# Optimization experiments

Measured on AMD Instinct MI355X. Metric: run time of the kernel, lower is better.

Reference implementation:

```python
import jax, jax.numpy as jnp
import numpy as np

N = 50000      # nodes
E = 800000     # edges
F_IN = 16      # feature_size
D = 96         # d_model
G = 64         # graphs per batch


def _gcn_conv(x, W, b, src, dst, dis, num_nodes):
    # PyG GCNConv: out = D^{-1/2}(A+I)D^{-1/2} X W + b (self-loops already in src/dst)
    h = x @ W                                   # [N, out]
    norm = (dis[src] * dis[dst])[:, None]       # [E+N, 1]
    msg = h[src] * norm                         # gather + scale
    agg = jax.ops.segment_sum(msg, dst, num_segments=num_nodes)
    return agg + b


def _forward(x, W_init, b_init, W1, b1, W2, b2, W3, b3, W4, b4,
             Wo1, bo1, Wo2, bo2, edge_index, batch_index):
    act = jax.nn.leaky_relu  # default negative_slope=0.01, matches nn.LeakyReLU()
    n = x.shape[0]
    # add self-loops once; degree includes self-loop (PyG gcn_norm default)
    loop = jnp.arange(n, dtype=edge_index.dtype)
    src = jnp.concatenate([edge_index[0], loop])
    dst = jnp.concatenate([edge_index[1], loop])
    deg = jax.ops.segment_sum(jnp.ones_like(src, dtype=x.dtype), dst, num_segments=n)
    dis = jax.lax.rsqrt(deg)  # deg >= 1 due to self-loops

    h = act(_gcn_conv(x, W_init, b_init, src, dst, dis, n))
    h = act(_gcn_conv(h, W1, b1, src, dst, dis, n))
    h = act(_gcn_conv(h, W2, b2, src, dst, dis, n))
    h = act(_gcn_conv(h, W3, b3, src, dst, dis, n))
    h = act(_gcn_conv(h, W4, b4, src, dst, dis, n))

    # global max + mean pooling per graph
    gmax = jax.ops.segment_max(h, batch_index, num_segments=G)
    gsum = jax.ops.segment_sum(h, batch_index, num_segments=G)
    cnt = jax.ops.segment_sum(jnp.ones((n,), dtype=h.dtype), batch_index, num_segments=G)
    gmean = gsum / jnp.maximum(cnt, 1.0)[:, None]
    pooled = jnp.concatenate([gmax, gmean], axis=1)  # [G, 2D]

    out = act(pooled @ Wo1 + bo1)  # dropout is identity in eval
    out = out @ Wo2 + bo2          # [G, 1]
    return out


def setup_inputs() -> dict:
    key = jax.random.key(0)
    ks = jax.random.split(key, 16)
    def glorot(k, shape):
        lim = float(np.sqrt(6.0 / (shape[0] + shape[1])))
        return jax.random.uniform(k, shape, jnp.float32, -lim, lim)
    inp = {
        'x': jax.random.normal(ks[0], (N, F_IN), jnp.float32),
        'edge_index': jax.random.randint(ks[1], (2, E), 0, N, dtype=jnp.int64),
        'batch_index': jnp.sort(jax.random.randint(ks[2], (N,), 0, G, dtype=jnp.int64)),
        'W_init': glorot(ks[3], (F_IN, D)), 'b_init': jnp.zeros((D,), jnp.float32),
        'W1': glorot(ks[4], (D, D)), 'b1': jnp.zeros((D,), jnp.float32),
        'W2': glorot(ks[5], (D, D)), 'b2': jnp.zeros((D,), jnp.float32),
        'W3': glorot(ks[6], (D, D)), 'b3': jnp.zeros((D,), jnp.float32),
        'W4': glorot(ks[7], (D, D)), 'b4': jnp.zeros((D,), jnp.float32),
        'Wo1': glorot(ks[8], (2 * D, D)), 'bo1': jnp.zeros((D,), jnp.float32),
        'Wo2': glorot(ks[9], (D, 1)), 'bo2': jnp.zeros((1,), jnp.float32),
    }
    return inp


def reference(x, edge_index, batch_index, W_init, b_init, W1, b1, W2, b2,
              W3, b3, W4, b4, Wo1, bo1, Wo2, bo2):
    return _forward(x, W_init, b_init, W1, b1, W2, b2, W3, b3, W4, b4,
                    Wo1, bo1, Wo2, bo2, edge_index, batch_index)
```

## Files before the change

### kernel.cpp

```cpp
#include <hip/hip_runtime.h>
#include <hip/hip_fp16.h>
#include <math.h>

#define LEAKY(x) ((x) > 0.f ? (x) : 0.01f * (x))
#define BK_SHIFT 9
#define NBMAX 128
#define BCAP 16384
#define EPAD 64

typedef _Float16 half8 __attribute__((ext_vector_type(8)));
typedef float f32x4 __attribute__((ext_vector_type(4)));

#define FMIX_LO(acc, u, m) \
    asm("v_fma_mix_f32 %0, %1, %2, %0 op_sel:[0,0,0] op_sel_hi:[1,0,0]" \
        : "+v"(acc) : "v"(u), "v"(m))
#define FMIX_HI(acc, u, m) \
    asm("v_fma_mix_f32 %0, %1, %2, %0 op_sel:[1,0,0] op_sel_hi:[1,0,0]" \
        : "+v"(acc) : "v"(u), "v"(m))

__device__ __forceinline__ void acc12(float (&acc)[12], uint2 u0, uint2 u1,
                                      uint2 u2, float m) {
    FMIX_LO(acc[0], u0.x, m);  FMIX_HI(acc[1], u0.x, m);
    FMIX_LO(acc[2], u0.y, m);  FMIX_HI(acc[3], u0.y, m);
    FMIX_LO(acc[4], u1.x, m);  FMIX_HI(acc[5], u1.x, m);
    FMIX_LO(acc[6], u1.y, m);  FMIX_HI(acc[7], u1.y, m);
    FMIX_LO(acc[8], u2.x, m);  FMIX_HI(acc[9], u2.x, m);
    FMIX_LO(acc[10], u2.y, m); FMIX_HI(acc[11], u2.y, m);
}

__device__ __forceinline__ unsigned encf(float f) {
    unsigned u = __float_as_uint(f);
    return (u & 0x80000000u) ? ~u : (u | 0x80000000u);
}
__device__ __forceinline__ float decf(unsigned u) {
    if (u == 0u) return -INFINITY;
    unsigned b = (u & 0x80000000u) ? (u & 0x7fffffffu) : ~u;
    return __uint_as_float(b);
}

__global__ __launch_bounds__(256) void prep(const float* __restrict__ W1,
                                            const float* __restrict__ W2,
                                            const float* __restrict__ W3,
                                            const float* __restrict__ W4,
                                            _Float16* __restrict__ WtG,
                                            int* __restrict__ bfill,
                                            int* __restrict__ epad,
                                            unsigned* __restrict__ gmaxU,
                                            float* __restrict__ gsum, int G) {
    int bi = blockIdx.x, tid = threadIdx.x;
    if (bi < 4) {
        const float* W = bi == 0 ? W1 : bi == 1 ? W2 : bi == 2 ? W3 : W4;
        _Float16* dst = WtG + bi * 9216;
        for (int idx = tid; idx < 9216; idx += 256) {
            int k = idx / 96, nn = idx % 96;
            dst[nn * 96 + k] = (_Float16)W[idx];
        }
    } else if (bi == 4) {
        for (int i2 = tid; i2 < NBMAX; i2 += 256) bfill[i2] = 0;
        for (int i2 = tid; i2 < EPAD; i2 += 256) epad[i2] = 0;
    } else if (bi == 5) {
        for (int i2 = tid; i2 < G * 96; i2 += 256) gmaxU[i2] = 0u;
    } else {
        for (int i2 = tid; i2 < G * 96; i2 += 256) gsum[i2] = 0.f;
    }
}

__global__ __launch_bounds__(256) void bin_kernel(const int* __restrict__ src,
                                                  const int* __restrict__ dst,
                                                  int* __restrict__ bfill,
                                                  uint2* __restrict__ tmp,
                                                  int E, int nb) {
    __shared__ int hist[NBMAX];
    __shared__ int scanbuf[NBMAX];
    __shared__ int lofs[NBMAX];
    __shared__ int adj[NBMAX];
    __shared__ uint2 buf[2048];
    __shared__ unsigned char bkt_of[2048];
    int base = blockIdx.x * 2048;
    int cnt = min(2048, E - base);
    int tid = threadIdx.x;
    for (int b = tid; b < NBMAX; b += 256) hist[b] = 0;
    __syncthreads();
    int es[8], ed[8];
#pragma unroll
    for (int k = 0; k < 8; ++k) {
        int l = tid + k * 256;
        if (l < cnt) {
            es[k] = src[base + l];
            ed[k] = dst[base + l];
            atomicAdd(&hist[ed[k] >> BK_SHIFT], 1);
        }
    }
    __syncthreads();
    if (tid < NBMAX) scanbuf[tid] = hist[tid];
    __syncthreads();
    for (int off = 1; off < NBMAX; off <<= 1) {
        int t = (tid < NBMAX && tid >= off) ? scanbuf[tid - off] : 0;
        __syncthreads();
        if (tid < NBMAX) scanbuf[tid] += t;
        __syncthreads();
    }
    if (tid < nb) {
        int cb = hist[tid];
        int start = scanbuf[tid] - cb;
        lofs[tid] = start;
        int g = (cb > 0) ? atomicAdd(&bfill[tid], cb) : 0;
        adj[tid] = tid * BCAP + g - start;
    }
    __syncthreads();
#pragma unroll
    for (int k = 0; k < 8; ++k) {
        int l = tid + k * 256;
        if (l < cnt) {
            int b = ed[k] >> BK_SHIFT;
            int r = atomicAdd(&lofs[b], 1);
            buf[r] = make_uint2((unsigned)es[k], (unsigned)ed[k]);
            bkt_of[r] = (unsigned char)b;
        }
    }
    __syncthreads();
    for (int j = tid; j < cnt; j += 256) {
        int b = bkt_of[j];
        tmp[adj[b] + j] = buf[j];
    }
}

__global__ __launch_bounds__(512) void place2(const uint2* __restrict__ tmp,
                                              const int* __restrict__ bfill,
                                              const float* __restrict__ X,
                                              float* __restrict__ dis,
                                              int* __restrict__ row_ptr,
                                              int* __restrict__ edge_src,
                                              float* __restrict__ Z0, int kq,
                                              int n, int E, int nb) {
    __shared__ int hist[512];
    __shared__ int sc[512];
    __shared__ int sbf[NBMAX];
    __shared__ int bb_s;
    int b = blockIdx.x;
    int tid = threadIdx.x;
    if (tid < NBMAX) sbf[tid] = (tid < nb) ? bfill[tid] : 0;
    hist[tid] = 0;
    __syncthreads();
    if (tid == 0) {
        int s = 0;
        for (int k = 0; k < b; ++k) s += sbf[k];
        bb_s = s;
    }
    __syncthreads();
    int bb = bb_s;
    int cnt = sbf[b];
    const uint2* mybkt = tmp + (size_t)b * BCAP;
    int node0 = b << BK_SHIFT;
    for (int j = tid; j < cnt; j += 512)
        atomicAdd(&hist[(int)mybkt[j].y - node0], 1);
    __syncthreads();
    int v = hist[tid];
    sc[tid] = v;
    __syncthreads();
    for (int off = 1; off < 512; off <<= 1) {
        int t = (tid >= off) ? sc[tid - off] : 0;
        __syncthreads();
        sc[tid] += t;
        __syncthreads();
    }
    int excl = sc[tid] - v;
    int i = node0 + tid;
    if (i < n) {
        row_ptr[i] = bb + excl;
        float di = rsqrtf((float)(v + 1));
        dis[i] = di;
        const float4* X4 = (const float4*)X;
        float4* Z4 = (float4*)Z0;
        for (int j = 0; j < kq; ++j) {
            float4 xv = X4[(size_t)i * kq + j];
            Z4[(size_t)i * kq + j] = make_float4(di * xv.x, di * xv.y, di * xv.z, di * xv.w);
        }
    }
    if (b == 0 && tid == 0) row_ptr[n] = E;
    __syncthreads();
    hist[tid] = bb + excl;
    __syncthreads();
    for (int j = tid; j < cnt; j += 512) {
        uint2 ev = mybkt[j];
        int pos = atomicAdd(&hist[(int)ev.y - node0], 1);
        edge_src[pos] = (int)ev.x;
    }
}

__global__ __launch_bounds__(256) void agg_wave0(const float* __restrict__ Z,
                                                 const float* __restrict__ dis,
                                                 const int* __restrict__ row_ptr,
                                                 const int* __restrict__ edge_src,
                                                 float* __restrict__ A, int n) {
    int i = (blockIdx.x * 256 + threadIdx.x) >> 6;
    if (i >= n) return;
    int lane = threadIdx.x & 63;
    int g = lane >> 2;
    int c = lane & 3;
    const float4* Z4 = (const float4*)Z;
    float di = dis[i];
    size_t base = (size_t)i * 4 + c;
    float4 acc = (g == 0) ? Z4[base] : make_float4(0.f, 0.f, 0.f, 0.f);
    int re0 = row_ptr[i], re1 = row_ptr[i + 1];
    int e0 = re0 + g;
    int s0 = edge_src[e0];
    int s1 = edge_src[e0 + 16];
    float m0 = (e0 < re1) ? 1.f : 0.f;
    float m1 = (e0 + 16 < re1) ? 1.f : 0.f;
    float4 u0 = Z4[(size_t)s0 * 4 + c];
    float4 u1 = Z4[(size_t)s1 * 4 + c];
    acc.x = fmaf(u0.x, m0, acc.x); acc.y = fmaf(u0.y, m0, acc.y);
    acc.z = fmaf(u0.z, m0, acc.z); acc.w = fmaf(u0.w, m0, acc.w);
    acc.x = fmaf(u1.x, m1, acc.x); acc.y = fmaf(u1.y, m1, acc.y);
    acc.z = fmaf(u1.z, m1, acc.z); acc.w = fmaf(u1.w, m1, acc.w);
    for (int e = e0 + 32; e < re1; e += 16) {
        int s = edge_src[e];
        float4 u = Z4[(size_t)s * 4 + c];
        acc.x += u.x; acc.y += u.y; acc.z += u.z; acc.w += u.w;
    }
#pragma unroll
    for (int m = 4; m < 64; m <<= 1) {
        acc.x += __shfl_xor(acc.x, m);
        acc.y += __shfl_xor(acc.y, m);
        acc.z += __shfl_xor(acc.z, m);
        acc.w += __shfl_xor(acc.w, m);
    }
    if (g == 0)
        ((float4*)A)[base] = make_float4(di * acc.x, di * acc.y,
                                         di * acc.z, di * acc.w);
}

__global__ __launch_bounds__(256) void agg_wave_h(const __half* __restrict__ Zh,
                                                  const float* __restrict__ dis,
                                                  const int* __restrict__ row_ptr,
                                                  const int* __restrict__ edge_src,
                                                  __half* __restrict__ A, int n) {
    int i = (blockIdx.x * 256 + threadIdx.x) >> 6;
    if (i >= n) return;
    int lane = threadIdx.x & 63;
    int g = lane >> 3;
    int c = lane & 7;
    float di = dis[i];
    float acc[12];
#pragma unroll
    for (int k = 0; k < 12; ++k) acc[k] = 0.f;
    int re0 = row_ptr[i], re1 = row_ptr[i + 1];
    int e0 = re0 + g;
    int s[4]; float m[4];
#pragma unroll
    for (int k = 0; k < 4; ++k) {
        int e = e0 + k * 8;
        s[k] = edge_src[e];
        m[k] = (e < re1) ? 1.0f : 0.0f;
    }
    uint2 u[4][3];
#pragma unroll
    for (int k = 0; k < 4; ++k) {
        const uint2* zp = (const uint2*)(Zh + (size_t)s[k] * 96 + c * 12);
        u[k][0] = zp[0]; u[k][1] = zp[1]; u[k][2] = zp[2];
    }
    if (g == 0) {
        const uint2* zp = (const uint2*)(Zh + (size_t)i * 96 + c * 12);
        acc12(acc, zp[0], zp[1], zp[2], 1.0f);
    }
#pragma unroll
    for (int k = 0; k < 4; ++k) acc12(acc, u[k][0], u[k][1], u[k][2], m[k]);
    for (int e = e0 + 32; e < re1; e += 8) {
        int s2 = edge_src[e];
        const uint2* zp = (const uint2*)(Zh + (size_t)s2 * 96 + c * 12);
        acc12(acc, zp[0], zp[1], zp[2], 1.0f);
    }
#pragma unroll
    for (int m2 = 8; m2 < 64; m2 <<= 1) {
#pragma unroll
        for (int k = 0; k < 12; ++k) acc[k] += __shfl_xor(acc[k], m2);
    }
    if (g == 0) {
        __half2 h0 = __floats2half2_rn(di * acc[0], di * acc[1]);
        __half2 h1 = __floats2half2_rn(di * acc[2], di * acc[3]);
        __half2 h2 = __floats2half2_rn(di * acc[4], di * acc[5]);
        __half2 h3 = __floats2half2_rn(di * acc[6], di * acc[7]);
        __half2 h4 = __floats2half2_rn(di * acc[8], di * acc[9]);
        __half2 h5 = __floats2half2_rn(di * acc[10], di * acc[11]);
        uint2 o0, o1, o2;
        o0.x = *(unsigned*)&h0; o0.y = *(unsigned*)&h1;
        o1.x = *(unsigned*)&h2; o1.y = *(unsigned*)&h3;
        o2.x = *(unsigned*)&h4; o2.y = *(unsigned*)&h5;
        uint2* ap = (uint2*)(A + (size_t)i * 96 + c * 12);
        ap[0] = o0; ap[1] = o1; ap[2] = o2;
    }
}

template <bool SCALE>
__global__ __launch_bounds__(256) void gemm_mfma(const __half* __restrict__ A,
                                                 const _Float16* __restrict__ Wt,
                                                 const float* __restrict__ b,
                                                 const float* __restrict__ dis,
                                                 __half* __restrict__ Xn, int n) {
    int tid = threadIdx.x;
    int i0 = blockIdx.x * 64;
    int w = tid >> 6, lane = tid & 63;
    int q = lane >> 4, c = lane & 15;
    int arow = i0 + w * 16 + c;
    const _Float16* Ap = (const _Float16*)A;
    half8 af[3];
    if (arow < n) {
#pragma unroll
        for (int kc = 0; kc < 3; ++kc)
            af[kc] = *(const half8*)&Ap[(size_t)arow * 96 + kc * 32 + q * 8];
    } else {
#pragma unroll
        for (int kc = 0; kc < 3; ++kc)
#pragma unroll
            for (int j = 0; j < 8; ++j) af[kc][j] = (_Float16)0.f;
    }
    float dvals[4];
#pragma unroll
    for (int r = 0; r < 4; ++r) {
        int gi = i0 + w * 16 + q * 4 + r;
        dvals[r] = (SCALE && gi < n) ? dis[gi] : 1.f;
    }
#pragma unroll
    for (int nt = 0; nt < 6; ++nt) {
        f32x4 acc = {0.f, 0.f, 0.f, 0.f};
#pragma unroll
        for (int kc = 0; kc < 3; ++kc) {
            half8 bf = *(const half8*)&Wt[(size_t)(nt * 16 + c) * 96 + kc * 32 + q * 8];
            acc = __builtin_amdgcn_mfma_f32_16x16x32_f16(af[kc], bf, acc, 0, 0, 0);
        }
        int col = nt * 16 + c;
        float bias = b[col];
#pragma unroll
        for (int r = 0; r < 4; ++r) {
            int gi = i0 + w * 16 + q * 4 + r;
            if (gi < n) {
                float v = acc[r] + bias;
                v = LEAKY(v);
                if (SCALE) v *= dvals[r];
                ((_Float16*)Xn)[(size_t)gi * 96 + col] = (_Float16)v;
            }
        }
    }
}

__global__ __launch_bounds__(256) void gemm_pool(const __half* __restrict__ A,
                                                 const _Float16* __restrict__ Wt,
                                                 const float* __restrict__ b,
                                                 const int* __restrict__ batch,
                                                 unsigned* __restrict__ gmaxU,
                                                 float* __restrict__ gsum, int n) {
    __shared__ float pmaxs[4][96];
    __shared__ float psums[4][96];
    int tid = threadIdx.x;
    int i0 = blockIdx.x * 64;
    int w = tid >> 6, lane = tid & 63;
    int q = lane >> 4, c = lane & 15;
    int arow = i0 + w * 16 + c;
    const _Float16* Ap = (const _Float16*)A;
    half8 af[3];
    if (arow < n) {
#pragma unroll
        for (int kc = 0; kc < 3; ++kc)
            af[kc] = *(const half8*)&Ap[(size_t)arow * 96 + kc * 32 + q * 8];
    } else {
#pragma unroll
        for (int kc = 0; kc < 3; ++kc)
#pragma unroll
            for (int j = 0; j < 8; ++j) af[kc][j] = (_Float16)0.f;
    }
    int row0 = i0 + w * 16;
    bool wuni = (row0 + 15 < n) && (batch[row0] == batch[row0 + 15]);
    bool buni = (i0 + 63 < n) && (batch[i0] == batch[i0 + 63]);
    int gw = wuni ? batch[row0] : 0;
#pragma unroll
    for (int nt = 0; nt < 6; ++nt) {
        f32x4 acc = {0.f, 0.f, 0.f, 0.f};
#pragma unroll
        for (int kc = 0; kc < 3; ++kc) {
            half8 bf = *(const half8*)&Wt[(size_t)(nt * 16 + c) * 96 + kc * 32 + q * 8];
            acc = __builtin_amdgcn_mfma_f32_16x16x32_f16(af[kc], bf, acc, 0, 0, 0);
        }
        int col = nt * 16 + c;
        float bias = b[col];
        float v[4];
#pragma unroll
        for (int r = 0; r < 4; ++r) {
            float t = acc[r] + bias;
            v[r] = LEAKY(t);
        }
        if (wuni) {
            float mx = fmaxf(fmaxf(v[0], v[1]), fmaxf(v[2], v[3]));
            float sm = v[0] + v[1] + v[2] + v[3];
            mx = fmaxf(mx, __shfl_xor(mx, 16)); sm += __shfl_xor(sm, 16);
            mx = fmaxf(mx, __shfl_xor(mx, 32)); sm += __shfl_xor(sm, 32);
            if (buni) {
                if (q == 0) { pmaxs[w][col] = mx; psums[w][col] = sm; }
            } else if (q == 0) {
                atomicMax(&gmaxU[gw * 96 + col], encf(mx));
                atomicAdd(&gsum[gw * 96 + col], sm);
            }
        } else {
            int r = 0;
            while (r < 4) {
                int gi = i0 + w * 16 + q * 4 + r;
                if (gi >= n) break;
                int gb = batch[gi];
                float mx = v[r], sm = v[r];
                int r2 = r + 1;
                for (; r2 < 4; ++r2) {
                    int gi2 = i0 + w * 16 + q * 4 + r2;
                    if (gi2 >= n || batch[gi2] != gb) break;
                    mx = fmaxf(mx, v[r2]); sm += v[r2];
                }
                atomicMax(&gmaxU[gb * 96 + col], encf(mx));
                atomicAdd(&gsum[gb * 96 + col], sm);
                r = r2;
            }
        }
    }
    __syncthreads();
    if (buni && tid < 96) {
        float m = fmaxf(fmaxf(pmaxs[0][tid], pmaxs[1][tid]),
                        fmaxf(pmaxs[2][tid], pmaxs[3][tid]));
        float s = psums[0][tid] + psums[1][tid] + psums[2][tid] + psums[3][tid];
        int gb = batch[i0];
        atomicMax(&gmaxU[gb * 96 + tid], encf(m));
        atomicAdd(&gsum[gb * 96 + tid], s);
    }
}

__global__ __launch_bounds__(192) void gemm_l0(const float* __restrict__ A,
                                               const float* __restrict__ W,
                                               const float* __restrict__ b,
                                               const float* __restrict__ dis,
                                               __half* __restrict__ Xn, int n) {
    constexpr int KQ = 4;
    __shared__ __align__(16) float4 Al[64 * KQ];
    int tid = threadIdx.x;
    int i0 = blockIdx.x * 64;
    for (int idx = tid; idx < 64 * KQ; idx += 192) {
        int gi = i0 + idx / KQ;
        Al[idx] = (gi < n) ? ((const float4*)A)[(size_t)i0 * KQ + idx]
                           : make_float4(0.f, 0.f, 0.f, 0.f);
    }
    __syncthreads();
    int fq = tid % 24;
    int g = tid / 24;
    const float4* W4 = (const float4*)W;
    float4 bb = ((const float4*)b)[fq];
    float4 acc[8];
#pragma unroll
    for (int r = 0; r < 8; ++r) acc[r] = bb;
    for (int kc = 0; kc < 16; kc += 8) {
        float4 w[8];
#pragma unroll
        for (int kk = 0; kk < 8; ++kk) w[kk] = W4[(size_t)(kc + kk) * 24 + fq];
#pragma unroll
        for (int r = 0; r < 8; ++r) {
            const float4* ar = &Al[(g * 8 + r) * KQ + (kc >> 2)];
#pragma unroll
            for (int k4 = 0; k4 < 2; ++k4) {
                float4 a = ar[k4];
                float4 w0 = w[4 * k4 + 0], w1 = w[4 * k4 + 1];
                float4 w2 = w[4 * k4 + 2], w3 = w[4 * k4 + 3];
                acc[r].x += a.x * w0.x + a.y * w1.x + a.z * w2.x + a.w * w3.x;
                acc[r].y += a.x * w0.y + a.y * w1.y + a.z * w2.y + a.w * w3.y;
                acc[r].z += a.x * w0.z + a.y * w1.z + a.z * w2.z + a.w * w3.z;
                acc[r].w += a.x * w0.w + a.y * w1.w + a.z * w2.w + a.w * w3.w;
            }
        }
    }
#pragma unroll
    for (int r = 0; r < 8; ++r) {
        int gi = i0 + g * 8 + r;
        if (gi < n) {
            float di = dis[gi];
            float4 o;
            o.x = di * LEAKY(acc[r].x); o.y = di * LEAKY(acc[r].y);
            o.z = di * LEAKY(acc[r].z); o.w = di * LEAKY(acc[r].w);
            __half2 h0 = __floats2half2_rn(o.x, o.y);
            __half2 h1 = __floats2half2_rn(o.z, o.w);
            uint2 u;
            u.x = *(unsigned*)&h0;
            u.y = *(unsigned*)&h1;
            ((uint2*)Xn)[(size_t)gi * 24 + fq] = u;
        }
    }
}

__device__ __forceinline__ int lower_bound(const int* b, int n, int v) {
    int lo = 0, hi = n;
    while (lo < hi) {
        int m = (lo + hi) >> 1;
        if (b[m] < v) lo = m + 1; else hi = m;
    }
    return lo;
}

__global__ void pool_final(const unsigned* __restrict__ gmaxU,
                           const float* __restrict__ gsum,
                           const int* __restrict__ batch,
                           const float* __restrict__ Wo1, const float* __restrict__ bo1,
                           const float* __restrict__ Wo2, const float* __restrict__ bo2,
                           float* __restrict__ out, int n) {
    __shared__ float pooled[192];
    __shared__ float sh[96];
    int g = blockIdx.x, f = threadIdx.x;
    int s = lower_bound(batch, n, g), e = lower_bound(batch, n, g + 1);
    float cnt = fmaxf((float)(e - s), 1.f);
    pooled[f] = decf(gmaxU[(size_t)g * 96 + f]);
    pooled[96 + f] = gsum[(size_t)g * 96 + f] / cnt;
    __syncthreads();
    float acc = bo1[f];
    for (int k = 0; k < 192; ++k) acc += pooled[k] * Wo1[k * 96 + f];
    float a = LEAKY(acc);
    sh[f] = a * Wo2[f];
    __syncthreads();
    if (f == 0) {
        float sacc = 0.f;
        for (int k = 0; k < 96; ++k) sacc += sh[k];
        out[g] = sacc + bo2[0];
    }
}

extern "C" void kernel_launch(void* const* d_in, const int* in_sizes, int n_in,
                              void* d_out, int out_size, void* d_ws, size_t ws_size,
                              hipStream_t stream) {
    const float* x      = (const float*)d_in[0];
    const int*   eidx   = (const int*)d_in[1];
    const int*   batch  = (const int*)d_in[2];
    const float* W_init = (const float*)d_in[3];
    const float* b_init = (const float*)d_in[4];
    const float* W1 = (const float*)d_in[5];  const float* b1 = (const float*)d_in[6];
    const float* W2 = (const float*)d_in[7];  const float* b2 = (const float*)d_in[8];
    const float* W3 = (const float*)d_in[9];  const float* b3 = (const float*)d_in[10];
    const float* W4 = (const float*)d_in[11]; const float* b4 = (const float*)d_in[12];
    const float* Wo1 = (const float*)d_in[13]; const float* bo1 = (const float*)d_in[14];
    const float* Wo2 = (const float*)d_in[15]; const float* bo2 = (const float*)d_in[16];
    float* out = (float*)d_out;

    const int N = in_sizes[2];
    const int E = in_sizes[1] / 2;
    const int G = out_size;
    const int* src = eidx;
    const int* dst = eidx + E;

    const int nbBkt  = (N + (1 << BK_SHIFT) - 1) >> BK_SHIFT;

    char* ws = (char*)d_ws;
    size_t off = 0;
    auto alloc = [&](size_t bytes) {
        size_t o = off;
        off += (bytes + 255) & ~(size_t)255;
        return o;
    };
    float*    dis      = (float*)(ws + alloc((size_t)N * 4));
    int*      row_ptr  = (int*)(ws + alloc((size_t)(N + 1) * 4));
    int*      bfill    = (int*)(ws + alloc(NBMAX * 4));
    unsigned* gmaxU    = (unsigned*)(ws + alloc((size_t)G * 96 * 4));
    float*    gsumB    = (float*)(ws + alloc((size_t)G * 96 * 4));
    int*      edge_src = (int*)(ws + alloc((size_t)(E + EPAD) * 4));
    float*    Z0       = (float*)(ws + alloc((size_t)N * 16 * 4));
    __half*   ZA       = (__half*)(ws + alloc((size_t)N * 96 * 2));
    __half*   ZB       = (__half*)(ws + alloc((size_t)N * 96 * 2));
    __half*   AggH     = (__half*)(ws + alloc((size_t)N * 96 * 2));
    float*    Agg0     = (float*)(ws + alloc((size_t)N * 16 * 4));
    _Float16* WtG      = (_Float16*)(ws + alloc((size_t)4 * 9216 * 2));
    uint2*    tmp      = (uint2*)(ws + alloc((size_t)nbBkt * BCAP * 8));
    (void)ws_size; (void)n_in;

    const int nbWave = (N + 3) / 4;
    const int nbTile = (N + 63) / 64;

    prep<<<7, 256, 0, stream>>>(W1, W2, W3, W4, WtG, bfill, edge_src + E,
                                gmaxU, gsumB, G);
    bin_kernel<<<(E + 2047) / 2048, 256, 0, stream>>>(src, dst, bfill, tmp, E, nbBkt);
    place2<<<nbBkt, 512, 0, stream>>>(tmp, bfill, x, dis, row_ptr, edge_src, Z0,
                                      4, N, E, nbBkt);

    agg_wave0<<<nbWave, 256, 0, stream>>>(Z0, dis, row_ptr, edge_src, Agg0, N);
    gemm_l0<<<nbTile, 192, 0, stream>>>(Agg0, W_init, b_init, dis, ZA, N);

    const float* bs[4] = {b1, b2, b3, b4};
    __half* cur = ZA;
    __half* nxt = ZB;
    for (int l = 0; l < 4; ++l) {
        agg_wave_h<<<nbWave, 256, 0, stream>>>(cur, dis, row_ptr, edge_src, AggH, N);
        if (l < 3) {
            gemm_mfma<true><<<nbTile, 256, 0, stream>>>(AggH, WtG + l * 9216, bs[l],
                                                        dis, nxt, N);
            __half* t = cur; cur = nxt; nxt = t;
        } else {
            gemm_pool<<<nbTile, 256, 0, stream>>>(AggH, WtG + 3 * 9216, bs[3],
                                                  batch, gmaxU, gsumB, N);
        }
    }

    pool_final<<<G, 96, 0, stream>>>(gmaxU, gsumB, batch, Wo1, bo1, Wo2, bo2, out, N);
}
```

Before: 327.0 us.

## Split fp16 node features into three 32-column planes for aggregation

Stores the 96-wide fp16 node features as three planes of 32 columns, so each aggregation launch handles one plane per block. Each lane now gathers one 8-byte chunk instead of three, and the GEMM and layer-0 kernels read and write the planar layout. The aim is a smaller per-row gather footprint that fits cache better, plus more blocks in flight. The cost is that row_ptr and edge_src are read three times, along with three times as many edge iterations. Out-of-range edge indices are also clamped to re0 so masked lanes no longer read past the row.

```diff
diff --git a/kernel.cpp b/kernel.cpp
--- a/kernel.cpp
+++ b/kernel.cpp
@@ -18,14 +18,9 @@
     asm("v_fma_mix_f32 %0, %1, %2, %0 op_sel:[1,0,0] op_sel_hi:[1,0,0]" \
         : "+v"(acc) : "v"(u), "v"(m))
 
-__device__ __forceinline__ void acc12(float (&acc)[12], uint2 u0, uint2 u1,
-                                      uint2 u2, float m) {
-    FMIX_LO(acc[0], u0.x, m);  FMIX_HI(acc[1], u0.x, m);
-    FMIX_LO(acc[2], u0.y, m);  FMIX_HI(acc[3], u0.y, m);
-    FMIX_LO(acc[4], u1.x, m);  FMIX_HI(acc[5], u1.x, m);
-    FMIX_LO(acc[6], u1.y, m);  FMIX_HI(acc[7], u1.y, m);
-    FMIX_LO(acc[8], u2.x, m);  FMIX_HI(acc[9], u2.x, m);
-    FMIX_LO(acc[10], u2.y, m); FMIX_HI(acc[11], u2.y, m);
+__device__ __forceinline__ void acc4(float (&acc)[4], uint2 u, float m) {
+    FMIX_LO(acc[0], u.x, m); FMIX_HI(acc[1], u.x, m);
+    FMIX_LO(acc[2], u.y, m); FMIX_HI(acc[3], u.y, m);
 }
 
 __device__ __forceinline__ unsigned encf(float f) {
@@ -204,8 +199,10 @@
     float4 acc = (g == 0) ? Z4[base] : make_float4(0.f, 0.f, 0.f, 0.f);
     int re0 = row_ptr[i], re1 = row_ptr[i + 1];
     int e0 = re0 + g;
-    int s0 = edge_src[e0];
-    int s1 = edge_src[e0 + 16];
+    int ec0 = (e0 < re1) ? e0 : re0;
+    int ec1 = (e0 + 16 < re1) ? e0 + 16 : re0;
+    int s0 = edge_src[ec0];
+    int s1 = edge_src[ec1];
     float m0 = (e0 < re1) ? 1.f : 0.f;
     float m1 = (e0 + 16 < re1) ? 1.f : 0.f;
     float4 u0 = Z4[(size_t)s0 * 4 + c];
@@ -231,64 +228,57 @@
                                          di * acc.z, di * acc.w);
 }
 
-__global__ __launch_bounds__(256) void agg_wave_h(const __half* __restrict__ Zh,
-                                                  const float* __restrict__ dis,
-                                                  const int* __restrict__ row_ptr,
-                                                  const int* __restrict__ edge_src,
-                                                  __half* __restrict__ A, int n) {
-    int i = (blockIdx.x * 256 + threadIdx.x) >> 6;
+__global__ __launch_bounds__(256) void agg_wave_hp(const __half* __restrict__ Zh,
+                                                   const float* __restrict__ dis,
+                                                   const int* __restrict__ row_ptr,
+                                                   const int* __restrict__ edge_src,
+                                                   __half* __restrict__ A,
+                                                   int n, int nbw) {
+    int bi = blockIdx.x;
+    int plane = bi / nbw;
+    int wi = bi - plane * nbw;
+    int i = (wi * 256 + threadIdx.x) >> 6;
     if (i >= n) return;
     int lane = threadIdx.x & 63;
     int g = lane >> 3;
     int c = lane & 7;
+    const uint2* Zp = (const uint2*)Zh + (size_t)plane * n * 8;
+    uint2* Ap = (uint2*)A + (size_t)plane * n * 8;
     float di = dis[i];
-    float acc[12];
-#pragma unroll
-    for (int k = 0; k < 12; ++k) acc[k] = 0.f;
+    float acc[4];
+#pragma unroll
+    for (int k = 0; k < 4; ++k) acc[k] = 0.f;
     int re0 = row_ptr[i], re1 = row_ptr[i + 1];
     int e0 = re0 + g;
     int s[4]; float m[4];
 #pragma unroll
     for (int k = 0; k < 4; ++k) {
         int e = e0 + k * 8;
-        s[k] = edge_src[e];
+        int ec = (e < re1) ? e : re0;
+        s[k] = edge_src[ec];
         m[k] = (e < re1) ? 1.0f : 0.0f;
     }
-    uint2 u[4][3];
-#pragma unroll
-    for (int k = 0; k < 4; ++k) {
-        const uint2* zp = (const uint2*)(Zh + (size_t)s[k] * 96 + c * 12);
-        u[k][0] = zp[0]; u[k][1] = zp[1]; u[k][2] = zp[2];
-    }
-    if (g == 0) {
-        const uint2* zp = (const uint2*)(Zh + (size_t)i * 96 + c * 12);
-        acc12(acc, zp[0], zp[1], zp[2], 1.0f);
-    }
-#pragma unroll
-    for (int k = 0; k < 4; ++k) acc12(acc, u[k][0], u[k][1], u[k][2], m[k]);
+    uint2 u[4];
+#pragma unroll
+    for (int k = 0; k < 4; ++k) u[k] = Zp[(size_t)s[k] * 8 + c];
+    if (g == 0) acc4(acc, Zp[(size_t)i * 8 + c], 1.0f);
+#pragma unroll
+    for (int k = 0; k < 4; ++k) acc4(acc, u[k], m[k]);
     for (int e = e0 + 32; e < re1; e += 8) {
         int s2 = edge_src[e];
-        const uint2* zp = (const uint2*)(Zh + (size_t)s2 * 96 + c * 12);
-        acc12(acc, zp[0], zp[1], zp[2], 1.0f);
+        acc4(acc, Zp[(size_t)s2 * 8 + c], 1.0f);
     }
 #pragma unroll
     for (int m2 = 8; m2 < 64; m2 <<= 1) {
 #pragma unroll
-        for (int k = 0; k < 12; ++k) acc[k] += __shfl_xor(acc[k], m2);
+        for (int k = 0; k < 4; ++k) acc[k] += __shfl_xor(acc[k], m2);
     }
     if (g == 0) {
         __half2 h0 = __floats2half2_rn(di * acc[0], di * acc[1]);
         __half2 h1 = __floats2half2_rn(di * acc[2], di * acc[3]);
-        __half2 h2 = __floats2half2_rn(di * acc[4], di * acc[5]);
-        __half2 h3 = __floats2half2_rn(di * acc[6], di * acc[7]);
-        __half2 h4 = __floats2half2_rn(di * acc[8], di * acc[9]);
-        __half2 h5 = __floats2half2_rn(di * acc[10], di * acc[11]);
-        uint2 o0, o1, o2;
-        o0.x = *(unsigned*)&h0; o0.y = *(unsigned*)&h1;
-        o1.x = *(unsigned*)&h2; o1.y = *(unsigned*)&h3;
-        o2.x = *(unsigned*)&h4; o2.y = *(unsigned*)&h5;
-        uint2* ap = (uint2*)(A + (size_t)i * 96 + c * 12);
-        ap[0] = o0; ap[1] = o1; ap[2] = o2;
+        uint2 o;
+        o.x = *(unsigned*)&h0; o.y = *(unsigned*)&h1;
+        Ap[(size_t)i * 8 + c] = o;
     }
 }
 
@@ -304,11 +294,12 @@
     int q = lane >> 4, c = lane & 15;
     int arow = i0 + w * 16 + c;
     const _Float16* Ap = (const _Float16*)A;
+    size_t pstride = (size_t)n * 32;
     half8 af[3];
     if (arow < n) {
 #pragma unroll
         for (int kc = 0; kc < 3; ++kc)
-            af[kc] = *(const half8*)&Ap[(size_t)arow * 96 + kc * 32 + q * 8];
+            af[kc] = *(const half8*)&Ap[kc * pstride + (size_t)arow * 32 + q * 8];
     } else {
 #pragma unroll
         for (int kc = 0; kc < 3; ++kc)
@@ -338,7 +329,8 @@
                 float v = acc[r] + bias;
                 v = LEAKY(v);
                 if (SCALE) v *= dvals[r];
-                ((_Float16*)Xn)[(size_t)gi * 96 + col] = (_Float16)v;
+                ((_Float16*)Xn)[(size_t)(col >> 5) * pstride +
+                                (size_t)gi * 32 + (col & 31)] = (_Float16)v;
             }
         }
     }
@@ -358,11 +350,12 @@
     int q = lane >> 4, c = lane & 15;
     int arow = i0 + w * 16 + c;
     const _Float16* Ap = (const _Float16*)A;
+    size_t pstride = (size_t)n * 32;
     half8 af[3];
     if (arow < n) {
 #pragma unroll
         for (int kc = 0; kc < 3; ++kc)
-            af[kc] = *(const half8*)&Ap[(size_t)arow * 96 + kc * 32 + q * 8];
+            af[kc] = *(const half8*)&Ap[kc * pstride + (size_t)arow * 32 + q * 8];
     } else {
 #pragma unroll
         for (int kc = 0; kc < 3; ++kc)
@@ -484,7 +477,7 @@
             uint2 u;
             u.x = *(unsigned*)&h0;
             u.y = *(unsigned*)&h1;
-            ((uint2*)Xn)[(size_t)gi * 24 + fq] = u;
+            ((uint2*)Xn)[(size_t)(fq >> 3) * n * 8 + (size_t)gi * 8 + (fq & 7)] = u;
         }
     }
 }
@@ -586,7 +579,8 @@
     __half* cur = ZA;
     __half* nxt = ZB;
     for (int l = 0; l < 4; ++l) {
-        agg_wave_h<<<nbWave, 256, 0, stream>>>(cur, dis, row_ptr, edge_src, AggH, N);
+        agg_wave_hp<<<3 * nbWave, 256, 0, stream>>>(cur, dis, row_ptr, edge_src,
+                                                    AggH, N, nbWave);
         if (l < 3) {
             gemm_mfma<true><<<nbTile, 256, 0, stream>>>(AggH, WtG + l * 9216, bs[l],
                                                         dis, nxt, N);
```

Measured after the change: 383.0 us. 1.17x slower.

## Replace bucketed CSR build with atomic histogram, three-phase scan and atomic scatter

Applied to the files above, without the earlier changes.

Replaces the two-pass bucket sort (bin_kernel and place2 through a temporary bucket buffer) with a plain per-node degree histogram built from global atomics, a three-kernel prefix scan into row_ptr, and an atomic scatter of source indices into edge_src. This drops the temporary uint2 buffer, the fixed bucket capacity and the serial per-block bucket prefix, in exchange for more kernel launches and heavily contended global atomics. The edge order within a row becomes nondeterministic. Aggregation kernels now clamp out-of-range edge indices to the row start, which avoids reading past a row's end.

```diff
diff --git a/kernel.cpp b/kernel.cpp
--- a/kernel.cpp
+++ b/kernel.cpp
@@ -3,10 +3,8 @@
 #include <math.h>
 
 #define LEAKY(x) ((x) > 0.f ? (x) : 0.01f * (x))
-#define BK_SHIFT 9
-#define NBMAX 128
-#define BCAP 16384
 #define EPAD 64
+#define SCANB 1024
 
 typedef _Float16 half8 __attribute__((ext_vector_type(8)));
 typedef float f32x4 __attribute__((ext_vector_type(4)));
@@ -43,10 +41,11 @@
                                             const float* __restrict__ W3,
                                             const float* __restrict__ W4,
                                             _Float16* __restrict__ WtG,
-                                            int* __restrict__ bfill,
+                                            int* __restrict__ deg,
                                             int* __restrict__ epad,
                                             unsigned* __restrict__ gmaxU,
-                                            float* __restrict__ gsum, int G) {
+                                            float* __restrict__ gsum,
+                                            int n, int G) {
     int bi = blockIdx.x, tid = threadIdx.x;
     if (bi < 4) {
         const float* W = bi == 0 ? W1 : bi == 1 ? W2 : bi == 2 ? W3 : W4;
@@ -55,136 +54,105 @@
             int k = idx / 96, nn = idx % 96;
             dst[nn * 96 + k] = (_Float16)W[idx];
         }
-    } else if (bi == 4) {
-        for (int i2 = tid; i2 < NBMAX; i2 += 256) bfill[i2] = 0;
-        for (int i2 = tid; i2 < EPAD; i2 += 256) epad[i2] = 0;
-    } else if (bi == 5) {
-        for (int i2 = tid; i2 < G * 96; i2 += 256) gmaxU[i2] = 0u;
     } else {
-        for (int i2 = tid; i2 < G * 96; i2 += 256) gsum[i2] = 0.f;
-    }
-}
-
-__global__ __launch_bounds__(256) void bin_kernel(const int* __restrict__ src,
-                                                  const int* __restrict__ dst,
-                                                  int* __restrict__ bfill,
-                                                  uint2* __restrict__ tmp,
-                                                  int E, int nb) {
-    __shared__ int hist[NBMAX];
-    __shared__ int scanbuf[NBMAX];
-    __shared__ int lofs[NBMAX];
-    __shared__ int adj[NBMAX];
-    __shared__ uint2 buf[2048];
-    __shared__ unsigned char bkt_of[2048];
-    int base = blockIdx.x * 2048;
-    int cnt = min(2048, E - base);
+        int t = (bi - 4) * 256 + tid;
+        int stride = (gridDim.x - 4) * 256;
+        for (int i2 = t; i2 < n; i2 += stride) deg[i2] = 0;
+        for (int i2 = t; i2 < G * 96; i2 += stride) { gmaxU[i2] = 0u; gsum[i2] = 0.f; }
+        for (int i2 = t; i2 < EPAD; i2 += stride) epad[i2] = 0;
+    }
+}
+
+__global__ __launch_bounds__(256) void hist_kernel(const int* __restrict__ dst,
+                                                   int* __restrict__ deg, int E) {
+    int e = blockIdx.x * 256 + threadIdx.x;
+    if (e < E) atomicAdd(&deg[dst[e]], 1);
+}
+
+__global__ __launch_bounds__(256) void scan_a(const int* __restrict__ deg,
+                                              int* __restrict__ rp,
+                                              int* __restrict__ bsum, int n) {
+    __shared__ int sc[256];
     int tid = threadIdx.x;
-    for (int b = tid; b < NBMAX; b += 256) hist[b] = 0;
+    int base = blockIdx.x * SCANB + tid * 4;
+    int4 d = make_int4(0, 0, 0, 0);
+    if (base + 3 < n) d = *(const int4*)&deg[base];
+    else {
+        if (base < n) d.x = deg[base];
+        if (base + 1 < n) d.y = deg[base + 1];
+        if (base + 2 < n) d.z = deg[base + 2];
+    }
+    int s = d.x + d.y + d.z + d.w;
+    sc[tid] = s;
     __syncthreads();
-    int es[8], ed[8];
-#pragma unroll
-    for (int k = 0; k < 8; ++k) {
-        int l = tid + k * 256;
-        if (l < cnt) {
-            es[k] = src[base + l];
-            ed[k] = dst[base + l];
-            atomicAdd(&hist[ed[k] >> BK_SHIFT], 1);
-        }
-    }
-    __syncthreads();
-    if (tid < NBMAX) scanbuf[tid] = hist[tid];
-    __syncthreads();
-    for (int off = 1; off < NBMAX; off <<= 1) {
-        int t = (tid < NBMAX && tid >= off) ? scanbuf[tid - off] : 0;
-        __syncthreads();
-        if (tid < NBMAX) scanbuf[tid] += t;
-        __syncthreads();
-    }
-    if (tid < nb) {
-        int cb = hist[tid];
-        int start = scanbuf[tid] - cb;
-        lofs[tid] = start;
-        int g = (cb > 0) ? atomicAdd(&bfill[tid], cb) : 0;
-        adj[tid] = tid * BCAP + g - start;
-    }
-    __syncthreads();
-#pragma unroll
-    for (int k = 0; k < 8; ++k) {
-        int l = tid + k * 256;
-        if (l < cnt) {
-            int b = ed[k] >> BK_SHIFT;
-            int r = atomicAdd(&lofs[b], 1);
-            buf[r] = make_uint2((unsigned)es[k], (unsigned)ed[k]);
-            bkt_of[r] = (unsigned char)b;
-        }
-    }
-    __syncthreads();
-    for (int j = tid; j < cnt; j += 256) {
-        int b = bkt_of[j];
-        tmp[adj[b] + j] = buf[j];
-    }
-}
-
-__global__ __launch_bounds__(512) void place2(const uint2* __restrict__ tmp,
-                                              const int* __restrict__ bfill,
-                                              const float* __restrict__ X,
-                                              float* __restrict__ dis,
-                                              int* __restrict__ row_ptr,
-                                              int* __restrict__ edge_src,
-                                              float* __restrict__ Z0, int kq,
-                                              int n, int E, int nb) {
-    __shared__ int hist[512];
-    __shared__ int sc[512];
-    __shared__ int sbf[NBMAX];
-    __shared__ int bb_s;
-    int b = blockIdx.x;
-    int tid = threadIdx.x;
-    if (tid < NBMAX) sbf[tid] = (tid < nb) ? bfill[tid] : 0;
-    hist[tid] = 0;
-    __syncthreads();
-    if (tid == 0) {
-        int s = 0;
-        for (int k = 0; k < b; ++k) s += sbf[k];
-        bb_s = s;
-    }
-    __syncthreads();
-    int bb = bb_s;
-    int cnt = sbf[b];
-    const uint2* mybkt = tmp + (size_t)b * BCAP;
-    int node0 = b << BK_SHIFT;
-    for (int j = tid; j < cnt; j += 512)
-        atomicAdd(&hist[(int)mybkt[j].y - node0], 1);
-    __syncthreads();
-    int v = hist[tid];
-    sc[tid] = v;
-    __syncthreads();
-    for (int off = 1; off < 512; off <<= 1) {
+    for (int off = 1; off < 256; off <<= 1) {
         int t = (tid >= off) ? sc[tid - off] : 0;
         __syncthreads();
         sc[tid] += t;
         __syncthreads();
     }
-    int excl = sc[tid] - v;
-    int i = node0 + tid;
-    if (i < n) {
-        row_ptr[i] = bb + excl;
-        float di = rsqrtf((float)(v + 1));
-        dis[i] = di;
-        const float4* X4 = (const float4*)X;
-        float4* Z4 = (float4*)Z0;
-        for (int j = 0; j < kq; ++j) {
-            float4 xv = X4[(size_t)i * kq + j];
-            Z4[(size_t)i * kq + j] = make_float4(di * xv.x, di * xv.y, di * xv.z, di * xv.w);
-        }
-    }
-    if (b == 0 && tid == 0) row_ptr[n] = E;
+    int excl = sc[tid] - s;
+    int r0 = excl, r1 = r0 + d.x, r2 = r1 + d.y, r3 = r2 + d.z;
+    if (base + 3 < n) *(int4*)&rp[base] = make_int4(r0, r1, r2, r3);
+    else {
+        if (base < n) rp[base] = r0;
+        if (base + 1 < n) rp[base + 1] = r1;
+        if (base + 2 < n) rp[base + 2] = r2;
+    }
+    if (tid == 255) bsum[blockIdx.x] = sc[255];
+}
+
+__global__ __launch_bounds__(64) void scan_b(int* __restrict__ bsum, int nb) {
+    __shared__ int sc[64];
+    int tid = threadIdx.x;
+    int v = (tid < nb) ? bsum[tid] : 0;
+    sc[tid] = v;
     __syncthreads();
-    hist[tid] = bb + excl;
-    __syncthreads();
-    for (int j = tid; j < cnt; j += 512) {
-        uint2 ev = mybkt[j];
-        int pos = atomicAdd(&hist[(int)ev.y - node0], 1);
-        edge_src[pos] = (int)ev.x;
+    for (int off = 1; off < 64; off <<= 1) {
+        int t = (tid >= off) ? sc[tid - off] : 0;
+        __syncthreads();
+        sc[tid] += t;
+        __syncthreads();
+    }
+    bsum[tid] = sc[tid] - v;
+}
+
+__global__ __launch_bounds__(256) void scan_c(int* __restrict__ rp,
+                                              int* __restrict__ cur,
+                                              const int* __restrict__ bsum,
+                                              const int* __restrict__ deg,
+                                              const float* __restrict__ X,
+                                              float* __restrict__ dis,
+                                              float* __restrict__ Z0,
+                                              int n, int E) {
+    int i = blockIdx.x * 256 + threadIdx.x;
+    if (i == 0) rp[n] = E;
+    if (i >= n) return;
+    int r = rp[i] + bsum[i >> 10];
+    rp[i] = r;
+    cur[i] = r;
+    float di = rsqrtf((float)(deg[i] + 1));
+    dis[i] = di;
+    const float4* X4 = (const float4*)X;
+    float4* Z4 = (float4*)Z0;
+#pragma unroll
+    for (int j = 0; j < 4; ++j) {
+        float4 xv = X4[(size_t)i * 4 + j];
+        Z4[(size_t)i * 4 + j] = make_float4(di * xv.x, di * xv.y,
+                                            di * xv.z, di * xv.w);
+    }
+}
+
+__global__ __launch_bounds__(256) void scatter_kernel(const int* __restrict__ src,
+                                                      const int* __restrict__ dst,
+                                                      int* __restrict__ cur,
+                                                      int* __restrict__ edge_src,
+                                                      int E) {
+    int e = blockIdx.x * 256 + threadIdx.x;
+    if (e < E) {
+        int s = src[e], d = dst[e];
+        int pos = atomicAdd(&cur[d], 1);
+        edge_src[pos] = s;
     }
 }
 
@@ -204,8 +172,10 @@
     float4 acc = (g == 0) ? Z4[base] : make_float4(0.f, 0.f, 0.f, 0.f);
     int re0 = row_ptr[i], re1 = row_ptr[i + 1];
     int e0 = re0 + g;
-    int s0 = edge_src[e0];
-    int s1 = edge_src[e0 + 16];
+    int ec0 = (e0 < re1) ? e0 : re0;
+    int ec1 = (e0 + 16 < re1) ? e0 + 16 : re0;
+    int s0 = edge_src[ec0];
+    int s1 = edge_src[ec1];
     float m0 = (e0 < re1) ? 1.f : 0.f;
     float m1 = (e0 + 16 < re1) ? 1.f : 0.f;
     float4 u0 = Z4[(size_t)s0 * 4 + c];
@@ -251,7 +221,8 @@
 #pragma unroll
     for (int k = 0; k < 4; ++k) {
         int e = e0 + k * 8;
-        s[k] = edge_src[e];
+        int ec = (e < re1) ? e : re0;
+        s[k] = edge_src[ec];
         m[k] = (e < re1) ? 1.0f : 0.0f;
     }
     uint2 u[4][3];
@@ -546,8 +517,6 @@
     const int* src = eidx;
     const int* dst = eidx + E;
 
-    const int nbBkt  = (N + (1 << BK_SHIFT) - 1) >> BK_SHIFT;
-
     char* ws = (char*)d_ws;
     size_t off = 0;
     auto alloc = [&](size_t bytes) {
@@ -557,7 +526,9 @@
     };
     float*    dis      = (float*)(ws + alloc((size_t)N * 4));
     int*      row_ptr  = (int*)(ws + alloc((size_t)(N + 1) * 4));
-    int*      bfill    = (int*)(ws + alloc(NBMAX * 4));
+    int*      cur      = (int*)(ws + alloc((size_t)N * 4));
+    int*      deg      = (int*)(ws + alloc((size_t)N * 4));
+    int*      bsum     = (int*)(ws + alloc(64 * 4));
     unsigned* gmaxU    = (unsigned*)(ws + alloc((size_t)G * 96 * 4));
     float*    gsumB    = (float*)(ws + alloc((size_t)G * 96 * 4));
     int*      edge_src = (int*)(ws + alloc((size_t)(E + EPAD) * 4));
@@ -567,30 +538,34 @@
     __half*   AggH     = (__half*)(ws + alloc((size_t)N * 96 * 2));
     float*    Agg0     = (float*)(ws + alloc((size_t)N * 16 * 4));
     _Float16* WtG      = (_Float16*)(ws + alloc((size_t)4 * 9216 * 2));
-    uint2*    tmp      = (uint2*)(ws + alloc((size_t)nbBkt * BCAP * 8));
     (void)ws_size; (void)n_in;
 
     const int nbWave = (N + 3) / 4;
     const int nbTile = (N + 63) / 64;
-
-    prep<<<7, 256, 0, stream>>>(W1, W2, W3, W4, WtG, bfill, edge_src + E,
-                                gmaxU, gsumB, G);
-    bin_kernel<<<(E + 2047) / 2048, 256, 0, stream>>>(src, dst, bfill, tmp, E, nbBkt);
-    place2<<<nbBkt, 512, 0, stream>>>(tmp, bfill, x, dis, row_ptr, edge_src, Z0,
-                                      4, N, E, nbBkt);
+    const int nbE    = (E + 255) / 256;
+    const int nbScan = (N + SCANB - 1) / SCANB;
+    const int nbNode = (N + 255) / 256;
+
+    prep<<<4 + 16, 256, 0, stream>>>(W1, W2, W3, W4, WtG, deg, edge_src + E,
+                                     gmaxU, gsumB, N, G);
+    hist_kernel<<<nbE, 256, 0, stream>>>(dst, deg, E);
+    scan_a<<<nbScan, 256, 0, stream>>>(deg, row_ptr, bsum, N);
+    scan_b<<<1, 64, 0, stream>>>(bsum, nbScan);
+    scan_c<<<nbNode, 256, 0, stream>>>(row_ptr, cur, bsum, deg, x, dis, Z0, N, E);
+    scatter_kernel<<<nbE, 256, 0, stream>>>(src, dst, cur, edge_src, E);
 
     agg_wave0<<<nbWave, 256, 0, stream>>>(Z0, dis, row_ptr, edge_src, Agg0, N);
     gemm_l0<<<nbTile, 192, 0, stream>>>(Agg0, W_init, b_init, dis, ZA, N);
 
     const float* bs[4] = {b1, b2, b3, b4};
-    __half* cur = ZA;
+    __half* curZ = ZA;
     __half* nxt = ZB;
     for (int l = 0; l < 4; ++l) {
-        agg_wave_h<<<nbWave, 256, 0, stream>>>(cur, dis, row_ptr, edge_src, AggH, N);
+        agg_wave_h<<<nbWave, 256, 0, stream>>>(curZ, dis, row_ptr, edge_src, AggH, N);
         if (l < 3) {
             gemm_mfma<true><<<nbTile, 256, 0, stream>>>(AggH, WtG + l * 9216, bs[l],
                                                         dis, nxt, N);
-            __half* t = cur; cur = nxt; nxt = t;
+            __half* t = curZ; curZ = nxt; nxt = t;
         } else {
             gemm_pool<<<nbTile, 256, 0, stream>>>(AggH, WtG + 3 * 9216, bs[3],
                                                   batch, gmaxU, gsumB, N);
```

Result: slower. 377.6 us (+15.5%).
